# Kernel optimization log

Measured on AMD Instinct MI355X. Metric: run time of the kernel, lower is better.

Reference implementation:

```python
import jax, jax.numpy as jnp
import numpy as np

SCALE = float(np.sqrt(0.7))


def setup_inputs() -> dict:
    key = jax.random.key(0)
    ks = jax.random.split(key, 8)
    B, H, E, T, S = 8, 512, 256, 2048, 2048
    return {
        "dec_conved": jax.random.normal(ks[0], (B, H, T), dtype=jnp.float32),
        "embedd": jax.random.normal(ks[1], (B, T, E), dtype=jnp.float32),
        "en_conved": jax.random.normal(ks[2], (B, S, E), dtype=jnp.float32),
        "en_combined": jax.random.normal(ks[3], (B, S, E), dtype=jnp.float32),
        # nn.Linear params: W is [out, in], y = x @ W.T + b
        "W_h2e": jax.random.normal(ks[4], (E, H), dtype=jnp.float32) / np.sqrt(H),
        "b_h2e": jax.random.normal(ks[5], (E,), dtype=jnp.float32) * 0.01,
        "W_e2h": jax.random.normal(ks[6], (H, E), dtype=jnp.float32) / np.sqrt(E),
        "b_e2h": jax.random.normal(ks[7], (H,), dtype=jnp.float32) * 0.01,
    }


def reference(dec_conved, embedd, en_conved, en_combined, W_h2e, b_h2e, W_e2h, b_e2h):
    # dec_conved: [B, H, T] -> [B, T, H]
    dc = jnp.swapaxes(dec_conved, 1, 2)
    # hid2emb: [B, T, E]
    dc_emb = jnp.einsum('bth,eh->bte', dc, W_h2e) + b_h2e
    Q = (dc_emb + embedd) * SCALE  # [B, T, E]
    # energy: [B, T, S]
    energy = jnp.einsum('bte,bse->bts', Q, en_conved)
    a = jax.nn.softmax(energy, axis=2)
    # context: [B, T, E]
    context = jnp.einsum('bts,bse->bte', a, en_combined)
    # emb2hid: [B, T, H]
    context = jnp.einsum('bte,he->bth', context, W_e2h) + b_e2h
    conved = (context + dc) * SCALE  # [B, T, H]
    return (a, jnp.swapaxes(conved, 1, 2))
```

## Files before the change

kernel.cpp:

```cpp
#include <hip/hip_runtime.h>
#include <math.h>
#include <stdint.h>

#define B_ 8
#define H_ 512
#define E_ 256
#define T_ 2048
#define S_ 2048
static constexpr float SCALE = 0.83666002653407555f;
static constexpr float ESHIFT = 60.0f;

typedef _Float16 half8 __attribute__((ext_vector_type(8)));
typedef _Float16 half4v __attribute__((ext_vector_type(4)));
typedef short short8 __attribute__((ext_vector_type(8)));
typedef unsigned short ushort8v __attribute__((ext_vector_type(8)));
typedef unsigned short ushort4v __attribute__((ext_vector_type(4)));
typedef float f32x4 __attribute__((ext_vector_type(4)));

__device__ __forceinline__ unsigned short f2bf(float f) {
    unsigned int u = __float_as_uint(f);
    u += 0x7FFFu + ((u >> 16) & 1u);
    return (unsigned short)(u >> 16);
}
__device__ __forceinline__ float bf2f(unsigned short u) {
    return __uint_as_float(((unsigned int)u) << 16);
}

__device__ __forceinline__ void xcd_remap(int gx, int gy, int gz, int& x, int& y, int& z) {
    const int h = blockIdx.x + gx * (blockIdx.y + gy * blockIdx.z);
    const int nwg = gx * gy * gz;
    const int wid = (h & 7) * (nwg >> 3) + (h >> 3);
    x = wid % gx;
    y = (wid / gx) % gy;
    z = wid / (gx * gy);
}

__global__ __launch_bounds__(256) void k_cast_all(const float* __restrict__ enc,
                                                  const float* __restrict__ w1,
                                                  const float* __restrict__ w2,
                                                  _Float16* __restrict__ encK,
                                                  _Float16* __restrict__ W1b,
                                                  _Float16* __restrict__ W2b) {
    const int i = blockIdx.x * 256 + threadIdx.x;
    const int N1 = B_ * S_ * E_ / 8;
    const int N2 = E_ * H_ / 8;
    const float* src; _Float16* dst; int off;
    if (i < N1)            { src = enc; dst = encK; off = i; }
    else if (i < N1 + N2)  { src = w1;  dst = W1b;  off = i - N1; }
    else                   { src = w2;  dst = W2b;  off = i - N1 - N2; }
    const float4* p = (const float4*)(src + (size_t)off * 8);
    const float4 a = p[0], b = p[1];
    half8 v;
    v[0] = (_Float16)a.x; v[1] = (_Float16)a.y; v[2] = (_Float16)a.z; v[3] = (_Float16)a.w;
    v[4] = (_Float16)b.x; v[5] = (_Float16)b.y; v[6] = (_Float16)b.z; v[7] = (_Float16)b.w;
    *(half8*)(dst + (size_t)off * 8) = v;
}

__global__ __launch_bounds__(256) void k_tcast(const float* __restrict__ in,
                                               _Float16* __restrict__ out, int R, int C) {
    __shared__ float tile[32][33];
    const size_t nb = (size_t)R * C;
    const float* inb = in + (size_t)blockIdx.z * nb;
    _Float16* outb = out + (size_t)blockIdx.z * nb;
    const int c0 = blockIdx.x * 32, r0 = blockIdx.y * 32;
    const int tr = threadIdx.x >> 3;
    const int tc = (threadIdx.x & 7) * 4;
    const float4 v = *(const float4*)(inb + (size_t)(r0 + tr) * C + c0 + tc);
    tile[tr][tc + 0] = v.x; tile[tr][tc + 1] = v.y;
    tile[tr][tc + 2] = v.z; tile[tr][tc + 3] = v.w;
    __syncthreads();
    half4v o;
    o[0] = (_Float16)tile[tc + 0][tr]; o[1] = (_Float16)tile[tc + 1][tr];
    o[2] = (_Float16)tile[tc + 2][tr]; o[3] = (_Float16)tile[tc + 3][tr];
    *(half4v*)(outb + (size_t)(c0 + tr) * R + r0 + tc) = o;
}

__global__ __launch_bounds__(256) void k_tcast_bf(const float* __restrict__ in,
                                                  unsigned short* __restrict__ out, int R, int C) {
    __shared__ float tile[32][33];
    const size_t nb = (size_t)R * C;
    const float* inb = in + (size_t)blockIdx.z * nb;
    unsigned short* outb = out + (size_t)blockIdx.z * nb;
    const int c0 = blockIdx.x * 32, r0 = blockIdx.y * 32;
    const int tr = threadIdx.x >> 3;
    const int tc = (threadIdx.x & 7) * 4;
    const float4 v = *(const float4*)(inb + (size_t)(r0 + tr) * C + c0 + tc);
    tile[tr][tc + 0] = v.x; tile[tr][tc + 1] = v.y;
    tile[tr][tc + 2] = v.z; tile[tr][tc + 3] = v.w;
    __syncthreads();
    ushort4v o;
    o[0] = f2bf(tile[tc + 0][tr]); o[1] = f2bf(tile[tc + 1][tr]);
    o[2] = f2bf(tile[tc + 2][tr]); o[3] = f2bf(tile[tc + 3][tr]);
    *(ushort4v*)(outb + (size_t)(c0 + tr) * R + r0 + tc) = o;
}

__device__ __forceinline__ void gl_lds16(const _Float16* g, _Float16* l) {
    __builtin_amdgcn_global_load_lds(
        (const __attribute__((address_space(1))) void*)g,
        (__attribute__((address_space(3))) void*)l, 16, 0, 0);
}

__device__ __forceinline__ void stage64x32_gl(const _Float16* __restrict__ g, int ld,
                                              _Float16* __restrict__ lds, int wv, int l) {
    const int r = (wv << 4) + (l >> 2);
    const int c = (l & 3) << 3;
    gl_lds16(g + (size_t)r * ld + c, lds + (wv << 9));
}

__device__ __forceinline__ void stage128x32_gl(const _Float16* __restrict__ g, int ld,
                                               _Float16* __restrict__ lds, int wv, int l) {
    const int r = (wv << 4) + (l >> 2);
    const int c = (l & 3) << 3;
    gl_lds16(g + (size_t)r * ld + c, lds + (wv << 9));
    gl_lds16(g + (size_t)(r + 64) * ld + c, lds + ((wv + 4) << 9));
}

#define G64_PROLOG                                                      \
    __shared__ __align__(16) _Float16 Ash[2][64 * 32];                  \
    __shared__ __align__(16) _Float16 Bsh[2][64 * 32];                  \
    const int tid = threadIdx.x;                                        \
    const int lane = tid & 63, wv = tid >> 6;                           \
    const int wm = (wv >> 1) * 32, wn = (wv & 1) * 32;                  \
    const int fr = lane & 15, fk = (lane >> 4) * 8;                     \
    f32x4 acc[2][2] = {};

#define G64_STEP_F16(cur)                                               \
    {                                                                   \
        half8 af[2], bv[2];                                             \
        _Pragma("unroll")                                               \
        for (int i = 0; i < 2; ++i) {                                   \
            af[i] = *(const half8*)&Ash[cur][(wm + i * 16 + fr) * 32 + fk]; \
            bv[i] = *(const half8*)&Bsh[cur][(wn + i * 16 + fr) * 32 + fk]; \
        }                                                               \
        _Pragma("unroll")                                               \
        for (int mi = 0; mi < 2; ++mi)                                  \
            _Pragma("unroll")                                           \
            for (int ni = 0; ni < 2; ++ni)                              \
                acc[mi][ni] = __builtin_amdgcn_mfma_f32_16x16x32_f16(   \
                    af[mi], bv[ni], acc[mi][ni], 0, 0, 0);              \
    }

#define G64_STEP_BF16(cur)                                              \
    {                                                                   \
        short8 af[2], bv[2];                                            \
        _Pragma("unroll")                                               \
        for (int i = 0; i < 2; ++i) {                                   \
            af[i] = *(const short8*)&Ash[cur][(wm + i * 16 + fr) * 32 + fk]; \
            bv[i] = *(const short8*)&Bsh[cur][(wn + i * 16 + fr) * 32 + fk]; \
        }                                                               \
        _Pragma("unroll")                                               \
        for (int mi = 0; mi < 2; ++mi)                                  \
            _Pragma("unroll")                                           \
            for (int ni = 0; ni < 2; ++ni)                              \
                acc[mi][ni] = __builtin_amdgcn_mfma_f32_16x16x32_bf16(  \
                    af[mi], bv[ni], acc[mi][ni], 0, 0, 0);              \
    }

__global__ __launch_bounds__(256) void k_q64(const _Float16* __restrict__ decT,
                                             const _Float16* __restrict__ W1,
                                             const float* __restrict__ bias,
                                             const float* __restrict__ emb,
                                             _Float16* __restrict__ Qb) {
    G64_PROLOG
    int bx, by, b;
    xcd_remap(E_ / 64, T_ / 64, B_, bx, by, b);
    const int t0 = by * 64, e0 = bx * 64;
    const _Float16* Ab = decT + ((size_t)b * T_ + t0) * H_;
    const _Float16* Bb = W1 + (size_t)e0 * H_;
    stage64x32_gl(Ab, H_, Ash[0], wv, lane);
    stage64x32_gl(Bb, H_, Bsh[0], wv, lane);
    __syncthreads();
    const int NK = H_ / 32;
    for (int k = 0; k < NK; ++k) {
        const int cur = k & 1;
        if (k + 1 < NK) {
            stage64x32_gl(Ab + (k + 1) * 32, H_, Ash[cur ^ 1], wv, lane);
            stage64x32_gl(Bb + (k + 1) * 32, H_, Bsh[cur ^ 1], wv, lane);
        }
        G64_STEP_F16(cur)
        __syncthreads();
    }
    const int cr = (lane >> 4) * 4, cn = lane & 15;
    const float* embb = emb + (size_t)b * T_ * E_;
    _Float16* Qo = Qb + (size_t)b * T_ * E_;
#pragma unroll
    for (int mi = 0; mi < 2; ++mi)
#pragma unroll
        for (int r = 0; r < 4; ++r) {
            const int t = t0 + wm + mi * 16 + cr + r;
#pragma unroll
            for (int ni = 0; ni < 2; ++ni) {
                const int e = e0 + wn + ni * 16 + cn;
                const float v = (acc[mi][ni][r] + bias[e] + embb[(size_t)t * E_ + e]) * SCALE;
                Qo[(size_t)t * E_ + e] = (_Float16)v;
            }
        }
}

__global__ __launch_bounds__(256) void k_pexp(const _Float16* __restrict__ Qb,
                                              const _Float16* __restrict__ Kb,
                                              unsigned short* __restrict__ P,
                                              float* __restrict__ gpart) {
    __shared__ __align__(16) _Float16 Ash[2][128 * 32];
    __shared__ __align__(16) _Float16 Bsh[2][128 * 32];
    __shared__ float psh[128][2];
    const int tid = threadIdx.x, lane = tid & 63, wv = tid >> 6;
    const int wm = (wv >> 1) * 64, wn = (wv & 1) * 64;
    const int fr = lane & 15, fk = (lane >> 4) * 8;
    f32x4 acc[4][4] = {};
    int bx, by, b;
    xcd_remap(S_ / 128, T_ / 128, B_, bx, by, b);
    const int t0 = by * 128, s0 = bx * 128;
    const _Float16* Ab = Qb + ((size_t)b * T_ + t0) * E_;
    const _Float16* Bb = Kb + ((size_t)b * S_ + s0) * E_;
    stage128x32_gl(Ab, E_, Ash[0], wv, lane);
    stage128x32_gl(Bb, E_, Bsh[0], wv, lane);
    __syncthreads();
    const int NK = E_ / 32;
    for (int k = 0; k < NK; ++k) {
        const int cur = k & 1;
        if (k + 1 < NK) {
            stage128x32_gl(Ab + (k + 1) * 32, E_, Ash[cur ^ 1], wv, lane);
            stage128x32_gl(Bb + (k + 1) * 32, E_, Bsh[cur ^ 1], wv, lane);
        }
        {
            half8 af[4], bv[4];
#pragma unroll
            for (int i = 0; i < 4; ++i) {
                af[i] = *(const half8*)&Ash[cur][(wm + i * 16 + fr) * 32 + fk];
                bv[i] = *(const half8*)&Bsh[cur][(wn + i * 16 + fr) * 32 + fk];
            }
#pragma unroll
            for (int mi = 0; mi < 4; ++mi)
#pragma unroll
                for (int ni = 0; ni < 4; ++ni)
                    acc[mi][ni] = __builtin_amdgcn_mfma_f32_16x16x32_f16(
                        af[mi], bv[ni], acc[mi][ni], 0, 0, 0);
        }
        __syncthreads();
    }
    const int cr = (lane >> 4) * 4, cn = lane & 15;
    unsigned short* Pb = P + ((size_t)b * T_ + t0) * S_ + s0;
#pragma unroll
    for (int mi = 0; mi < 4; ++mi)
#pragma unroll
        for (int r = 0; r < 4; ++r) {
            const int tl = wm + mi * 16 + cr + r;
            float rs = 0.f;
#pragma unroll
            for (int ni = 0; ni < 4; ++ni) {
                const float p = __expf(acc[mi][ni][r] - ESHIFT);
                rs += p;
                Pb[(size_t)tl * S_ + wn + ni * 16 + cn] = f2bf(p);
            }
#pragma unroll
            for (int m = 1; m < 16; m <<= 1) rs += __shfl_xor(rs, m);
            if (cn == 0) psh[tl][wv & 1] = rs;
        }
    __syncthreads();
    if (tid < 128)
        gpart[((size_t)b * T_ + t0 + tid) * 16 + bx] = psh[tid][0] + psh[tid][1];
}

__global__ __launch_bounds__(256) void k_anorm(const unsigned short* __restrict__ P,
                                               const float* __restrict__ gpart,
                                               float* __restrict__ rinv,
                                               float* __restrict__ a) {
    const size_t row = blockIdx.x;
    __shared__ float sinv;
    const int tid = threadIdx.x;
    if (tid < 16) {
        float v = gpart[row * 16 + tid];
#pragma unroll
        for (int m = 1; m < 16; m <<= 1) v += __shfl_xor(v, m);
        if (tid == 0) {
            const float inv = 1.0f / v;
            sinv = inv;
            rinv[row] = inv;
        }
    }
    __syncthreads();
    const float inv = sinv;
    const unsigned short* p = P + row * (size_t)S_;
    float* o = a + row * (size_t)S_;
    const ushort8v v = *(const ushort8v*)(p + (size_t)tid * 8);
    float4 o0, o1;
    o0.x = bf2f(v[0]) * inv; o0.y = bf2f(v[1]) * inv;
    o0.z = bf2f(v[2]) * inv; o0.w = bf2f(v[3]) * inv;
    o1.x = bf2f(v[4]) * inv; o1.y = bf2f(v[5]) * inv;
    o1.z = bf2f(v[6]) * inv; o1.w = bf2f(v[7]) * inv;
    ((float4*)o)[tid * 2] = o0;
    ((float4*)o)[tid * 2 + 1] = o1;
}

__global__ __launch_bounds__(256) void k_ctx64(const _Float16* __restrict__ Pa,
                                               const _Float16* __restrict__ Vt,
                                               const float* __restrict__ rinv,
                                               _Float16* __restrict__ ctxb) {
    G64_PROLOG
    int bx, by, b;
    xcd_remap(E_ / 64, T_ / 64, B_, bx, by, b);
    const int t0 = by * 64, e0 = bx * 64;
    const _Float16* Ab = Pa + ((size_t)b * T_ + t0) * S_;
    const _Float16* Bb = Vt + ((size_t)b * E_ + e0) * S_;
    stage64x32_gl(Ab, S_, Ash[0], wv, lane);
    stage64x32_gl(Bb, S_, Bsh[0], wv, lane);
    __syncthreads();
    const int NK = S_ / 32;
    for (int k = 0; k < NK; ++k) {
        const int cur = k & 1;
        if (k + 1 < NK) {
            stage64x32_gl(Ab + (k + 1) * 32, S_, Ash[cur ^ 1], wv, lane);
            stage64x32_gl(Bb + (k + 1) * 32, S_, Bsh[cur ^ 1], wv, lane);
        }
        G64_STEP_BF16(cur)
        __syncthreads();
    }
    const int cr = (lane >> 4) * 4, cn = lane & 15;
    _Float16* co = ctxb + (size_t)b * T_ * E_;
    const float* rib = rinv + (size_t)b * T_;
#pragma unroll
    for (int mi = 0; mi < 2; ++mi)
#pragma unroll
        for (int r = 0; r < 4; ++r) {
            const int t = t0 + wm + mi * 16 + cr + r;
            const float inv = rib[t];
#pragma unroll
            for (int ni = 0; ni < 2; ++ni) {
                const int e = e0 + wn + ni * 16 + cn;
                co[(size_t)t * E_ + e] = (_Float16)(acc[mi][ni][r] * inv);
            }
        }
}

__global__ __launch_bounds__(256) void k_out64(const _Float16* __restrict__ W2,
                                               const _Float16* __restrict__ ctxb,
                                               const float* __restrict__ bias,
                                               const float* __restrict__ dec,
                                               float* __restrict__ out2) {
    G64_PROLOG
    int bx, by, b;
    xcd_remap(T_ / 64, H_ / 64, B_, bx, by, b);
    const int h0 = by * 64, t0 = bx * 64;
    const _Float16* Ab = W2 + (size_t)h0 * E_;
    const _Float16* Bb = ctxb + ((size_t)b * T_ + t0) * E_;
    stage64x32_gl(Ab, E_, Ash[0], wv, lane);
    stage64x32_gl(Bb, E_, Bsh[0], wv, lane);
    __syncthreads();
    const int NK = E_ / 32;
    for (int k = 0; k < NK; ++k) {
        const int cur = k & 1;
        if (k + 1 < NK) {
            stage64x32_gl(Ab + (k + 1) * 32, E_, Ash[cur ^ 1], wv, lane);
            stage64x32_gl(Bb + (k + 1) * 32, E_, Bsh[cur ^ 1], wv, lane);
        }
        G64_STEP_F16(cur)
        __syncthreads();
    }
    const int cr = (lane >> 4) * 4, cn = lane & 15;
    const float* decb = dec + (size_t)b * H_ * T_;
    float* ob = out2 + (size_t)b * H_ * T_;
#pragma unroll
    for (int mi = 0; mi < 2; ++mi)
#pragma unroll
        for (int r = 0; r < 4; ++r) {
            const int h = h0 + wm + mi * 16 + cr + r;
            const float bj = bias[h];
#pragma unroll
            for (int ni = 0; ni < 2; ++ni) {
                const int t = t0 + wn + ni * 16 + cn;
                const size_t idx = (size_t)h * T_ + t;
                ob[idx] = (acc[mi][ni][r] + bj + decb[idx]) * SCALE;
            }
        }
}

extern "C" void kernel_launch(void* const* d_in, const int* in_sizes, int n_in,
                              void* d_out, int out_size, void* d_ws, size_t ws_size,
                              hipStream_t stream) {
    const float* dec   = (const float*)d_in[0];
    const float* emb   = (const float*)d_in[1];
    const float* enc   = (const float*)d_in[2];
    const float* encc  = (const float*)d_in[3];
    const float* W_h2e = (const float*)d_in[4];
    const float* b_h2e = (const float*)d_in[5];
    const float* W_e2h = (const float*)d_in[6];
    const float* b_e2h = (const float*)d_in[7];

    float* a_out = (float*)d_out;
    float* out2  = a_out + (size_t)B_ * T_ * S_;

    _Float16* ws    = (_Float16*)d_ws;
    _Float16* decT  = ws;
    _Float16* encK  = decT + (size_t)B_ * T_ * H_;
    _Float16* enccT = encK + (size_t)B_ * S_ * E_;
    _Float16* W1b   = enccT + (size_t)B_ * S_ * E_;
    _Float16* W2b   = W1b + (size_t)E_ * H_;
    _Float16* Qb    = W2b + (size_t)H_ * E_;
    _Float16* ctxb  = Qb + (size_t)B_ * T_ * E_;
    _Float16* Pbuf  = ctxb + (size_t)B_ * T_ * E_;
    float*    gpart = (float*)(Pbuf + (size_t)B_ * T_ * S_);
    float*    rinv  = gpart + (size_t)B_ * T_ * 16;

    const dim3 blk(256);
    const int NCAST = (B_ * S_ * E_ / 8) + (E_ * H_ / 8) + (H_ * E_ / 8);
    k_cast_all<<<dim3(NCAST / 256), blk, 0, stream>>>(enc, W_h2e, W_e2h, encK, W1b, W2b);
    k_tcast   <<<dim3(T_ / 32, H_ / 32, B_), blk, 0, stream>>>(dec, decT, H_, T_);
    k_tcast_bf<<<dim3(E_ / 32, S_ / 32, B_), blk, 0, stream>>>(encc, (unsigned short*)enccT, S_, E_);
    k_q64  <<<dim3(E_ / 64, T_ / 64, B_),   blk, 0, stream>>>(decT, W1b, b_h2e, emb, Qb);
    k_pexp <<<dim3(S_ / 128, T_ / 128, B_), blk, 0, stream>>>(Qb, encK, (unsigned short*)Pbuf, gpart);
    k_anorm<<<dim3(B_ * T_),                blk, 0, stream>>>((const unsigned short*)Pbuf, gpart, rinv, a_out);
    k_ctx64<<<dim3(E_ / 64, T_ / 64, B_),   blk, 0, stream>>>(Pbuf, enccT, rinv, ctxb);
    k_out64<<<dim3(T_ / 64, H_ / 64, B_),   blk, 0, stream>>>(W2b, ctxb, b_e2h, dec, out2);
}
```

Baseline: 376.1 us.

## Fuse softmax normalization into context GEMM and merge prep kernels

Removes the standalone normalization kernel: the context GEMM now computes the row reciprocal sums from the partial sums and writes the normalized attention output from the P tile already staged in LDS. Each of the four E-blocks writes a distinct quarter of the S columns, so the bf16 P matrix no longer has to be read a second time from global memory. The three cast/transpose kernels are also merged into one launch to cut launch overhead. In exchange, the GEMM main loop now carries extra global stores that may slow it down.

```diff
diff --git a/kernel.cpp b/kernel.cpp
--- a/kernel.cpp
+++ b/kernel.cpp
@@ -35,63 +35,70 @@
     z = wid / (gx * gy);
 }
 
-__global__ __launch_bounds__(256) void k_cast_all(const float* __restrict__ enc,
-                                                  const float* __restrict__ w1,
-                                                  const float* __restrict__ w2,
-                                                  _Float16* __restrict__ encK,
-                                                  _Float16* __restrict__ W1b,
-                                                  _Float16* __restrict__ W2b) {
-    const int i = blockIdx.x * 256 + threadIdx.x;
-    const int N1 = B_ * S_ * E_ / 8;
-    const int N2 = E_ * H_ / 8;
-    const float* src; _Float16* dst; int off;
-    if (i < N1)            { src = enc; dst = encK; off = i; }
-    else if (i < N1 + N2)  { src = w1;  dst = W1b;  off = i - N1; }
-    else                   { src = w2;  dst = W2b;  off = i - N1 - N2; }
-    const float4* p = (const float4*)(src + (size_t)off * 8);
-    const float4 a = p[0], b = p[1];
-    half8 v;
-    v[0] = (_Float16)a.x; v[1] = (_Float16)a.y; v[2] = (_Float16)a.z; v[3] = (_Float16)a.w;
-    v[4] = (_Float16)b.x; v[5] = (_Float16)b.y; v[6] = (_Float16)b.z; v[7] = (_Float16)b.w;
-    *(half8*)(dst + (size_t)off * 8) = v;
-}
-
-__global__ __launch_bounds__(256) void k_tcast(const float* __restrict__ in,
-                                               _Float16* __restrict__ out, int R, int C) {
+__global__ __launch_bounds__(256) void k_prep(const float* __restrict__ enc,
+                                              const float* __restrict__ w1,
+                                              const float* __restrict__ w2,
+                                              const float* __restrict__ dec,
+                                              const float* __restrict__ encc,
+                                              _Float16* __restrict__ encK,
+                                              _Float16* __restrict__ W1b,
+                                              _Float16* __restrict__ W2b,
+                                              _Float16* __restrict__ decT,
+                                              unsigned short* __restrict__ enccT) {
+    constexpr int NC = (B_ * S_ * E_ / 8 + E_ * H_ / 8 + H_ * E_ / 8) / 256;
+    constexpr int NT1 = (T_ / 32) * (H_ / 32) * B_;
     __shared__ float tile[32][33];
-    const size_t nb = (size_t)R * C;
-    const float* inb = in + (size_t)blockIdx.z * nb;
-    _Float16* outb = out + (size_t)blockIdx.z * nb;
-    const int c0 = blockIdx.x * 32, r0 = blockIdx.y * 32;
-    const int tr = threadIdx.x >> 3;
-    const int tc = (threadIdx.x & 7) * 4;
-    const float4 v = *(const float4*)(inb + (size_t)(r0 + tr) * C + c0 + tc);
-    tile[tr][tc + 0] = v.x; tile[tr][tc + 1] = v.y;
-    tile[tr][tc + 2] = v.z; tile[tr][tc + 3] = v.w;
-    __syncthreads();
-    half4v o;
-    o[0] = (_Float16)tile[tc + 0][tr]; o[1] = (_Float16)tile[tc + 1][tr];
-    o[2] = (_Float16)tile[tc + 2][tr]; o[3] = (_Float16)tile[tc + 3][tr];
-    *(half4v*)(outb + (size_t)(c0 + tr) * R + r0 + tc) = o;
-}
-
-__global__ __launch_bounds__(256) void k_tcast_bf(const float* __restrict__ in,
-                                                  unsigned short* __restrict__ out, int R, int C) {
-    __shared__ float tile[32][33];
-    const size_t nb = (size_t)R * C;
-    const float* inb = in + (size_t)blockIdx.z * nb;
-    unsigned short* outb = out + (size_t)blockIdx.z * nb;
-    const int c0 = blockIdx.x * 32, r0 = blockIdx.y * 32;
-    const int tr = threadIdx.x >> 3;
-    const int tc = (threadIdx.x & 7) * 4;
-    const float4 v = *(const float4*)(inb + (size_t)(r0 + tr) * C + c0 + tc);
-    tile[tr][tc + 0] = v.x; tile[tr][tc + 1] = v.y;
-    tile[tr][tc + 2] = v.z; tile[tr][tc + 3] = v.w;
-    __syncthreads();
-    ushort4v o;
-    o[0] = f2bf(tile[tc + 0][tr]); o[1] = f2bf(tile[tc + 1][tr]);
-    o[2] = f2bf(tile[tc + 2][tr]); o[3] = f2bf(tile[tc + 3][tr]);
-    *(ushort4v*)(outb + (size_t)(c0 + tr) * R + r0 + tc) = o;
+    const int gb = blockIdx.x;
+    const int tid = threadIdx.x;
+    if (gb < NC) {
+        const int i = gb * 256 + tid;
+        const int N1 = B_ * S_ * E_ / 8;
+        const int N2 = E_ * H_ / 8;
+        const float* src; _Float16* dst; int off;
+        if (i < N1)           { src = enc; dst = encK; off = i; }
+        else if (i < N1 + N2) { src = w1;  dst = W1b;  off = i - N1; }
+        else                  { src = w2;  dst = W2b;  off = i - N1 - N2; }
+        const float4* p = (const float4*)(src + (size_t)off * 8);
+        const float4 a = p[0], b = p[1];
+        half8 v;
+        v[0] = (_Float16)a.x; v[1] = (_Float16)a.y; v[2] = (_Float16)a.z; v[3] = (_Float16)a.w;
+        v[4] = (_Float16)b.x; v[5] = (_Float16)b.y; v[6] = (_Float16)b.z; v[7] = (_Float16)b.w;
+        *(half8*)(dst + (size_t)off * 8) = v;
+        return;
+    }
+    const int tr = tid >> 3;
+    const int tc = (tid & 7) * 4;
+    if (gb < NC + NT1) {
+        const int l = gb - NC;
+        const int bx = l & 63, by = (l >> 6) & 15, bz = l >> 10;
+        const int c0 = bx * 32, r0 = by * 32;
+        const float* inb = dec + (size_t)bz * H_ * T_;
+        _Float16* outb = decT + (size_t)bz * T_ * H_;
+        const float4 v = *(const float4*)(inb + (size_t)(r0 + tr) * T_ + c0 + tc);
+        tile[tr][tc + 0] = v.x; tile[tr][tc + 1] = v.y;
+        tile[tr][tc + 2] = v.z; tile[tr][tc + 3] = v.w;
+        __syncthreads();
+        half4v o;
+        o[0] = (_Float16)tile[tc + 0][tr]; o[1] = (_Float16)tile[tc + 1][tr];
+        o[2] = (_Float16)tile[tc + 2][tr]; o[3] = (_Float16)tile[tc + 3][tr];
+        *(half4v*)(outb + (size_t)(c0 + tr) * H_ + r0 + tc) = o;
+        return;
+    }
+    {
+        const int l = gb - NC - NT1;
+        const int bx = l & 7, by = (l >> 3) & 63, bz = l >> 9;
+        const int c0 = bx * 32, r0 = by * 32;
+        const float* inb = encc + (size_t)bz * S_ * E_;
+        unsigned short* outb = enccT + (size_t)bz * E_ * S_;
+        const float4 v = *(const float4*)(inb + (size_t)(r0 + tr) * E_ + c0 + tc);
+        tile[tr][tc + 0] = v.x; tile[tr][tc + 1] = v.y;
+        tile[tr][tc + 2] = v.z; tile[tr][tc + 3] = v.w;
+        __syncthreads();
+        ushort4v o;
+        o[0] = f2bf(tile[tc + 0][tr]); o[1] = f2bf(tile[tc + 1][tr]);
+        o[2] = f2bf(tile[tc + 2][tr]); o[3] = f2bf(tile[tc + 3][tr]);
+        *(ushort4v*)(outb + (size_t)(c0 + tr) * S_ + r0 + tc) = o;
+    }
 }
 
 __device__ __forceinline__ void gl_lds16(const _Float16* g, _Float16* l) {
@@ -262,42 +269,13 @@
         gpart[((size_t)b * T_ + t0 + tid) * 16 + bx] = psh[tid][0] + psh[tid][1];
 }
 
-__global__ __launch_bounds__(256) void k_anorm(const unsigned short* __restrict__ P,
-                                               const float* __restrict__ gpart,
-                                               float* __restrict__ rinv,
-                                               float* __restrict__ a) {
-    const size_t row = blockIdx.x;
-    __shared__ float sinv;
-    const int tid = threadIdx.x;
-    if (tid < 16) {
-        float v = gpart[row * 16 + tid];
-#pragma unroll
-        for (int m = 1; m < 16; m <<= 1) v += __shfl_xor(v, m);
-        if (tid == 0) {
-            const float inv = 1.0f / v;
-            sinv = inv;
-            rinv[row] = inv;
-        }
-    }
-    __syncthreads();
-    const float inv = sinv;
-    const unsigned short* p = P + row * (size_t)S_;
-    float* o = a + row * (size_t)S_;
-    const ushort8v v = *(const ushort8v*)(p + (size_t)tid * 8);
-    float4 o0, o1;
-    o0.x = bf2f(v[0]) * inv; o0.y = bf2f(v[1]) * inv;
-    o0.z = bf2f(v[2]) * inv; o0.w = bf2f(v[3]) * inv;
-    o1.x = bf2f(v[4]) * inv; o1.y = bf2f(v[5]) * inv;
-    o1.z = bf2f(v[6]) * inv; o1.w = bf2f(v[7]) * inv;
-    ((float4*)o)[tid * 2] = o0;
-    ((float4*)o)[tid * 2 + 1] = o1;
-}
-
 __global__ __launch_bounds__(256) void k_ctx64(const _Float16* __restrict__ Pa,
                                                const _Float16* __restrict__ Vt,
-                                               const float* __restrict__ rinv,
+                                               const float* __restrict__ gpart,
+                                               float* __restrict__ a_out,
                                                _Float16* __restrict__ ctxb) {
     G64_PROLOG
+    __shared__ float rinv_sh[64];
     int bx, by, b;
     xcd_remap(E_ / 64, T_ / 64, B_, bx, by, b);
     const int t0 = by * 64, e0 = bx * 64;
@@ -305,7 +283,17 @@
     const _Float16* Bb = Vt + ((size_t)b * E_ + e0) * S_;
     stage64x32_gl(Ab, S_, Ash[0], wv, lane);
     stage64x32_gl(Bb, S_, Bsh[0], wv, lane);
+    if (tid < 64) {
+        const float* gp = gpart + ((size_t)b * T_ + t0 + tid) * 16;
+        float s = 0.f;
+#pragma unroll
+        for (int i = 0; i < 16; ++i) s += gp[i];
+        rinv_sh[tid] = 1.0f / s;
+    }
     __syncthreads();
+    const int ar = tid >> 2, ac = (tid & 3) * 8;
+    const float ainv = rinv_sh[ar];
+    float* arow = a_out + ((size_t)b * T_ + t0 + ar) * S_ + ac;
     const int NK = S_ / 32;
     for (int k = 0; k < NK; ++k) {
         const int cur = k & 1;
@@ -314,21 +302,30 @@
             stage64x32_gl(Bb + (k + 1) * 32, S_, Bsh[cur ^ 1], wv, lane);
         }
         G64_STEP_BF16(cur)
+        if ((k >> 4) == bx) {
+            const ushort8v pv = *(const ushort8v*)&Ash[cur][ar * 32 + ac];
+            float4 w0, w1;
+            w0.x = bf2f(pv[0]) * ainv; w0.y = bf2f(pv[1]) * ainv;
+            w0.z = bf2f(pv[2]) * ainv; w0.w = bf2f(pv[3]) * ainv;
+            w1.x = bf2f(pv[4]) * ainv; w1.y = bf2f(pv[5]) * ainv;
+            w1.z = bf2f(pv[6]) * ainv; w1.w = bf2f(pv[7]) * ainv;
+            ((float4*)(arow + k * 32))[0] = w0;
+            ((float4*)(arow + k * 32))[1] = w1;
+        }
         __syncthreads();
     }
     const int cr = (lane >> 4) * 4, cn = lane & 15;
     _Float16* co = ctxb + (size_t)b * T_ * E_;
-    const float* rib = rinv + (size_t)b * T_;
 #pragma unroll
     for (int mi = 0; mi < 2; ++mi)
 #pragma unroll
         for (int r = 0; r < 4; ++r) {
-            const int t = t0 + wm + mi * 16 + cr + r;
-            const float inv = rib[t];
+            const int tl = wm + mi * 16 + cr + r;
+            const float inv = rinv_sh[tl];
 #pragma unroll
             for (int ni = 0; ni < 2; ++ni) {
                 const int e = e0 + wn + ni * 16 + cn;
-                co[(size_t)t * E_ + e] = (_Float16)(acc[mi][ni][r] * inv);
+                co[(size_t)(t0 + tl) * E_ + e] = (_Float16)(acc[mi][ni][r] * inv);
             }
         }
 }
@@ -400,16 +397,16 @@
     _Float16* ctxb  = Qb + (size_t)B_ * T_ * E_;
     _Float16* Pbuf  = ctxb + (size_t)B_ * T_ * E_;
     float*    gpart = (float*)(Pbuf + (size_t)B_ * T_ * S_);
-    float*    rinv  = gpart + (size_t)B_ * T_ * 16;
 
     const dim3 blk(256);
-    const int NCAST = (B_ * S_ * E_ / 8) + (E_ * H_ / 8) + (H_ * E_ / 8);
-    k_cast_all<<<dim3(NCAST / 256), blk, 0, stream>>>(enc, W_h2e, W_e2h, encK, W1b, W2b);
-    k_tcast   <<<dim3(T_ / 32, H_ / 32, B_), blk, 0, stream>>>(dec, decT, H_, T_);
-    k_tcast_bf<<<dim3(E_ / 32, S_ / 32, B_), blk, 0, stream>>>(encc, (unsigned short*)enccT, S_, E_);
+    constexpr int NPREP = (B_ * S_ * E_ / 8 + E_ * H_ / 8 + H_ * E_ / 8) / 256
+                        + (T_ / 32) * (H_ / 32) * B_
+                        + (E_ / 32) * (S_ / 32) * B_;
+    k_prep <<<dim3(NPREP),                 blk, 0, stream>>>(enc, W_h2e, W_e2h, dec, encc,
+                                                             encK, W1b, W2b, decT,
+                                                             (unsigned short*)enccT);
     k_q64  <<<dim3(E_ / 64, T_ / 64, B_),   blk, 0, stream>>>(decT, W1b, b_h2e, emb, Qb);
     k_pexp <<<dim3(S_ / 128, T_ / 128, B_), blk, 0, stream>>>(Qb, encK, (unsigned short*)Pbuf, gpart);
-    k_anorm<<<dim3(B_ * T_),                blk, 0, stream>>>((const unsigned short*)Pbuf, gpart, rinv, a_out);
-    k_ctx64<<<dim3(E_ / 64, T_ / 64, B_),   blk, 0, stream>>>(Pbuf, enccT, rinv, ctxb);
+    k_ctx64<<<dim3(E_ / 64, T_ / 64, B_),   blk, 0, stream>>>(Pbuf, enccT, gpart, a_out, ctxb);
     k_out64<<<dim3(T_ / 64, H_ / 64, B_),   blk, 0, stream>>>(W2b, ctxb, b_e2h, dec, out2);
 }
```

Result: faster. 367.7 us (-2.2%).
